# Optimization experiments

Hardware: AMD Instinct MI355X
Metric: run time of the kernel (lower is better)

The kernel has to match this reference:

```python
import jax, jax.numpy as jnp
import numpy as np

NEG_SLOPE = 0.2


def _gat_layer(x, src, dst, W, a_src, a_dst, b, n_nodes):
    # x: [N, Fin] -> h: [N, Fout]
    h = x @ W
    alpha_src = h @ a_src  # [N]
    alpha_dst = h @ a_dst  # [N]
    # per-edge attention logits (gather) + leaky relu
    e = jax.nn.leaky_relu(alpha_src[src] + alpha_dst[dst], negative_slope=NEG_SLOPE)
    # numerically-stable segment softmax over incoming edges of each dst node
    e_max = jax.ops.segment_max(e, dst, num_segments=n_nodes)
    e_exp = jnp.exp(e - e_max[dst])
    denom = jax.ops.segment_sum(e_exp, dst, num_segments=n_nodes)
    alpha = e_exp / denom[dst]  # every node has a self-loop, denom > 0
    # weighted scatter-aggregate of source features
    out = jax.ops.segment_sum(alpha[:, None] * h[src], dst, num_segments=n_nodes)
    return out + b


def setup_inputs() -> dict:
    N, E, D_EMB, D_HID = 100000, 1600000, 64, 64
    key = jax.random.key(0)
    ks = jax.random.split(key, 10)
    inp = {
        "prop_edge_index": jax.random.randint(ks[0], (2, E), 0, N, dtype=jnp.int64
                                              if jax.config.jax_enable_x64 else jnp.int32),
        "embedding": jax.random.normal(ks[1], (N, D_EMB), jnp.float32),
        "W1": jax.random.normal(ks[2], (D_EMB, D_HID), jnp.float32) / np.sqrt(D_EMB),
        "a1_src": jax.random.normal(ks[3], (D_HID,), jnp.float32) / np.sqrt(D_HID),
        "a1_dst": jax.random.normal(ks[4], (D_HID,), jnp.float32) / np.sqrt(D_HID),
        "b1": jnp.zeros((D_HID,), jnp.float32),
        "W2": jax.random.normal(ks[5], (D_HID, D_HID), jnp.float32) / np.sqrt(D_HID),
        "a2_src": jax.random.normal(ks[6], (D_HID,), jnp.float32) / np.sqrt(D_HID),
        "a2_dst": jax.random.normal(ks[7], (D_HID,), jnp.float32) / np.sqrt(D_HID),
        "b2": jnp.zeros((D_HID,), jnp.float32),
    }
    return inp


def reference(prop_edge_index, embedding, W1, a1_src, a1_dst, b1, W2, a2_src, a2_dst, b2):
    n_nodes = embedding.shape[0]
    # PyG GATConv adds self-loops by default
    loop = jnp.arange(n_nodes, dtype=prop_edge_index.dtype)
    src = jnp.concatenate([prop_edge_index[0], loop])
    dst = jnp.concatenate([prop_edge_index[1], loop])
    # dropout is identity in eval mode (args.training=False)
    x = embedding
    x = jax.nn.elu(_gat_layer(x, src, dst, W1, a1_src, a1_dst, b1, n_nodes))
    x = _gat_layer(x, src, dst, W2, a2_src, a2_dst, b2, n_nodes)
    return x
```

## Files before the change

### kernel.cpp

```cpp
#include <hip/hip_runtime.h>
#include <math.h>

#define D 64
#define NEG_SLOPE 0.2f
#define TILE 4096
#define BKT 128

__device__ __forceinline__ float lrelu(float x) { return fmaxf(x, NEG_SLOPE * x); }

__device__ __forceinline__ unsigned short f2bf(float f) {
    unsigned u = __float_as_uint(f);
    return (unsigned short)((u + 0x7fffu + ((u >> 16) & 1u)) >> 16);
}
__device__ __forceinline__ float2 bf2f2(unsigned u) {
    float2 r;
    r.x = __uint_as_float(u << 16);
    r.y = __uint_as_float(u & 0xffff0000u);
    return r;
}

__global__ __launch_bounds__(256, 4) void gemm_alpha(
    const float* __restrict__ x, const float* __restrict__ W,
    const float* __restrict__ a_src, const float* __restrict__ a_dst,
    unsigned short* __restrict__ hb, float* __restrict__ asrc,
    float* __restrict__ adst, int N) {
    __shared__ float xs[64][68];
    __shared__ float Ws[64][68];
    const int tid = threadIdx.x;
    const int r0 = blockIdx.x * 64;

    for (int i = tid; i < 4096; i += 256) {
        int k = i >> 6, c = i & 63;
        Ws[k][c] = W[i];
    }
    for (int i = tid; i < 4096; i += 256) {
        int r = i >> 6, k = i & 63;
        int gr = r0 + r;
        xs[r][k] = (gr < N) ? x[(size_t)gr * D + k] : 0.f;
    }
    __syncthreads();

    const int tx = tid & 15;
    const int ty = tid >> 4;
    float acc[4][4] = {};
#pragma unroll 4
    for (int k = 0; k < 64; k += 4) {
        float xr[4][4], wc[4][4];
#pragma unroll
        for (int i = 0; i < 4; ++i)
            *(float4*)xr[i] = *(const float4*)&xs[ty * 4 + i][k];
#pragma unroll
        for (int u = 0; u < 4; ++u)
            *(float4*)wc[u] = *(const float4*)&Ws[k + u][tx * 4];
#pragma unroll
        for (int i = 0; i < 4; ++i)
#pragma unroll
            for (int j = 0; j < 4; ++j)
#pragma unroll
                for (int u = 0; u < 4; ++u)
                    acc[i][j] = fmaf(xr[i][u], wc[u][j], acc[i][j]);
    }

#pragma unroll
    for (int i = 0; i < 4; ++i) {
        int gr = r0 + ty * 4 + i;
        if (gr < N) {
            uint2 p;
            p.x = (unsigned)f2bf(acc[i][0]) | ((unsigned)f2bf(acc[i][1]) << 16);
            p.y = (unsigned)f2bf(acc[i][2]) | ((unsigned)f2bf(acc[i][3]) << 16);
            *(uint2*)&hb[(size_t)gr * D + tx * 4] = p;
        }
    }
    float as4[4], ad4[4];
    *(float4*)as4 = *(const float4*)&a_src[tx * 4];
    *(float4*)ad4 = *(const float4*)&a_dst[tx * 4];
#pragma unroll
    for (int i = 0; i < 4; ++i) {
        float ps = 0.f, pd = 0.f;
#pragma unroll
        for (int j = 0; j < 4; ++j) {
            ps = fmaf(acc[i][j], as4[j], ps);
            pd = fmaf(acc[i][j], ad4[j], pd);
        }
#pragma unroll
        for (int off = 1; off < 16; off <<= 1) {
            ps += __shfl_xor(ps, off);
            pd += __shfl_xor(pd, off);
        }
        if (tx == 0) {
            int gr = r0 + ty * 4 + i;
            if (gr < N) { asrc[gr] = ps; adst[gr] = pd; }
        }
    }
}

__global__ void histA(const int* __restrict__ dst, int* __restrict__ mat,
                      int E, int nblkA, int NBc) {
    __shared__ int cnt[1024];
    for (int b = threadIdx.x; b < NBc; b += 256) cnt[b] = 0;
    __syncthreads();
    const int base = blockIdx.x * TILE;
    for (int j = threadIdx.x; j < TILE; j += 256) {
        int i = base + j;
        if (i < E) atomicAdd(&cnt[dst[i] >> 7], 1);
    }
    __syncthreads();
    for (int b = threadIdx.x; b < NBc; b += 256) mat[b * nblkA + blockIdx.x] = cnt[b];
}

__global__ void scan_part1(const int* __restrict__ a, int* __restrict__ bsum, int M) {
    __shared__ int s[4];
    const int lane = threadIdx.x & 63, wid = threadIdx.x >> 6;
    int base = blockIdx.x * 1024;
    int v = 0;
    for (int j = threadIdx.x; j < 1024; j += 256) {
        int i = base + j;
        v += (i < M) ? a[i] : 0;
    }
#pragma unroll
    for (int off = 32; off; off >>= 1) v += __shfl_xor(v, off);
    if (lane == 0) s[wid] = v;
    __syncthreads();
    if (threadIdx.x == 0) bsum[blockIdx.x] = s[0] + s[1] + s[2] + s[3];
}
__global__ void scan_part2(int* __restrict__ bsum, int nb) {
    const int lane = threadIdx.x;
    int running = 0;
    for (int base = 0; base < nb; base += 64) {
        int i = base + lane;
        int v = (i < nb) ? bsum[i] : 0;
        int x = v;
#pragma unroll
        for (int off = 1; off < 64; off <<= 1) {
            int y = __shfl_up(x, off);
            if (lane >= off) x += y;
        }
        if (i < nb) bsum[i] = running + x - v;
        running += __shfl(x, 63);
    }
}
__global__ void scan_part3(int* __restrict__ a, const int* __restrict__ bsum, int M) {
    __shared__ int wsum[4];
    const int lane = threadIdx.x & 63, wid = threadIdx.x >> 6;
    const int i0 = blockIdx.x * 1024 + (int)threadIdx.x * 4;
    int v[4];
#pragma unroll
    for (int u = 0; u < 4; ++u) v[u] = (i0 + u < M) ? a[i0 + u] : 0;
    int tsum = v[0] + v[1] + v[2] + v[3];
    int incl = tsum;
#pragma unroll
    for (int off = 1; off < 64; off <<= 1) {
        int y = __shfl_up(incl, off);
        if (lane >= off) incl += y;
    }
    if (lane == 63) wsum[wid] = incl;
    __syncthreads();
    int woff = 0;
    for (int w = 0; w < wid; ++w) woff += wsum[w];
    int ex = bsum[blockIdx.x] + woff + incl - tsum;
#pragma unroll
    for (int u = 0; u < 4; ++u) {
        if (i0 + u < M) a[i0 + u] = ex;
        ex += v[u];
    }
}

__global__ void scatterA(const int* __restrict__ src, const int* __restrict__ dst,
                         const int* __restrict__ mat, unsigned* __restrict__ tmp,
                         int E, int nblkA, int NBc) {
    __shared__ int cur[1024];
    for (int b = threadIdx.x; b < NBc; b += 256) cur[b] = mat[b * nblkA + blockIdx.x];
    __syncthreads();
    const int base = blockIdx.x * TILE;
    for (int j = threadIdx.x; j < TILE; j += 256) {
        int i = base + j;
        if (i < E) {
            int d = dst[i];
            int pos = atomicAdd(&cur[d >> 7], 1);
            tmp[pos] = ((unsigned)(d & (BKT - 1)) << 17) | (unsigned)src[i];
        }
    }
}

__global__ void bucket_build(const int* __restrict__ mat, const unsigned* __restrict__ tmp,
                             int* __restrict__ row, int* __restrict__ csr,
                             int N, int E, int nblkA, int NBc) {
    __shared__ int cnt[BKT];
    __shared__ int cur[BKT];
    __shared__ int wsumS[2];
    const int b = blockIdx.x;
    const int n0 = b << 7;
    const int tid = threadIdx.x;
    const int beg = mat[b * nblkA];
    const int end = (b + 1 < NBc) ? mat[(b + 1) * nblkA] : E;
    if (tid < BKT) cnt[tid] = 0;
    __syncthreads();
    for (int i = beg + tid; i < end; i += 256) atomicAdd(&cnt[tmp[i] >> 17], 1);
    __syncthreads();
    int v = (tid < BKT) ? cnt[tid] : 0;
    int x = v;
#pragma unroll
    for (int off = 1; off < 64; off <<= 1) {
        int y = __shfl_up(x, off);
        if ((tid & 63) >= off) x += y;
    }
    if (tid < BKT && (tid & 63) == 63) wsumS[tid >> 6] = x;
    __syncthreads();
    const int add = (tid >= 64 && tid < BKT) ? wsumS[0] : 0;
    const int ex = beg + add + x - v;
    if (tid < BKT) {
        const int node = n0 + tid;
        if (node < N) row[node] = ex;
        cur[tid] = ex;
    }
    if (b == NBc - 1 && tid == 0) row[N] = E;
    __syncthreads();
    for (int i = beg + tid; i < end; i += 256) {
        unsigned e = tmp[i];
        int pos = atomicAdd(&cur[e >> 17], 1);
        csr[pos] = (int)(e & 0x1FFFFu);
    }
}

__global__ __launch_bounds__(256) void aggregate(
    const int* __restrict__ row, const int* __restrict__ csr_src,
    const float* __restrict__ asrc, const float* __restrict__ adst,
    const unsigned short* __restrict__ hb, const float* __restrict__ bias,
    float* __restrict__ out, int N, int do_elu) {
    const int g = threadIdx.x >> 3;
    const int c = threadIdx.x & 7;
    const int d = blockIdx.x * 32 + g;
    if (d >= N) return;
    const int beg = row[d], end = row[d + 1];
    const float ad = adst[d];
    float dnp = __expf(lrelu(asrc[d] + ad));

    const unsigned short* hrow = hb + (c << 3);
    float acc[8];
    {
        const uint4 hv = *(const uint4*)(hrow + ((unsigned)d << 6));
        float2 p;
        p = bf2f2(hv.x); acc[0] = dnp * p.x; acc[1] = dnp * p.y;
        p = bf2f2(hv.y); acc[2] = dnp * p.x; acc[3] = dnp * p.y;
        p = bf2f2(hv.z); acc[4] = dnp * p.x; acc[5] = dnp * p.y;
        p = bf2f2(hv.w); acc[6] = dnp * p.x; acc[7] = dnp * p.y;
    }

    int i = beg;
    for (; i + 2 <= end; i += 2) {
        const int s0 = csr_src[i], s1 = csr_src[i + 1];
        const float a0 = asrc[s0], a1 = asrc[s1];
        const uint4 h0 = *(const uint4*)(hrow + ((unsigned)s0 << 6));
        const uint4 h1 = *(const uint4*)(hrow + ((unsigned)s1 << 6));
        const float w0 = __expf(lrelu(a0 + ad));
        const float w1 = __expf(lrelu(a1 + ad));
        dnp += w0 + w1;
        float2 p;
        p = bf2f2(h0.x); acc[0] = fmaf(w0, p.x, acc[0]); acc[1] = fmaf(w0, p.y, acc[1]);
        p = bf2f2(h0.y); acc[2] = fmaf(w0, p.x, acc[2]); acc[3] = fmaf(w0, p.y, acc[3]);
        p = bf2f2(h0.z); acc[4] = fmaf(w0, p.x, acc[4]); acc[5] = fmaf(w0, p.y, acc[5]);
        p = bf2f2(h0.w); acc[6] = fmaf(w0, p.x, acc[6]); acc[7] = fmaf(w0, p.y, acc[7]);
        p = bf2f2(h1.x); acc[0] = fmaf(w1, p.x, acc[0]); acc[1] = fmaf(w1, p.y, acc[1]);
        p = bf2f2(h1.y); acc[2] = fmaf(w1, p.x, acc[2]); acc[3] = fmaf(w1, p.y, acc[3]);
        p = bf2f2(h1.z); acc[4] = fmaf(w1, p.x, acc[4]); acc[5] = fmaf(w1, p.y, acc[5]);
        p = bf2f2(h1.w); acc[6] = fmaf(w1, p.x, acc[6]); acc[7] = fmaf(w1, p.y, acc[7]);
    }
    if (i < end) {
        const int s0 = csr_src[i];
        const float w0 = __expf(lrelu(asrc[s0] + ad));
        const uint4 h0 = *(const uint4*)(hrow + ((unsigned)s0 << 6));
        dnp += w0;
        float2 p;
        p = bf2f2(h0.x); acc[0] = fmaf(w0, p.x, acc[0]); acc[1] = fmaf(w0, p.y, acc[1]);
        p = bf2f2(h0.y); acc[2] = fmaf(w0, p.x, acc[2]); acc[3] = fmaf(w0, p.y, acc[3]);
        p = bf2f2(h0.z); acc[4] = fmaf(w0, p.x, acc[4]); acc[5] = fmaf(w0, p.y, acc[5]);
        p = bf2f2(h0.w); acc[6] = fmaf(w0, p.x, acc[6]); acc[7] = fmaf(w0, p.y, acc[7]);
    }

    const float inv = 1.f / dnp;
    const float4 b0 = *(const float4*)&bias[c << 3];
    const float4 b1 = *(const float4*)&bias[(c << 3) + 4];
    float v[8];
    v[0] = fmaf(acc[0], inv, b0.x); v[1] = fmaf(acc[1], inv, b0.y);
    v[2] = fmaf(acc[2], inv, b0.z); v[3] = fmaf(acc[3], inv, b0.w);
    v[4] = fmaf(acc[4], inv, b1.x); v[5] = fmaf(acc[5], inv, b1.y);
    v[6] = fmaf(acc[6], inv, b1.z); v[7] = fmaf(acc[7], inv, b1.w);
    if (do_elu) {
#pragma unroll
        for (int k = 0; k < 8; ++k) v[k] = v[k] > 0.f ? v[k] : expm1f(v[k]);
    }
    *(float4*)&out[((size_t)d << 6) + (c << 3)]     = *(float4*)&v[0];
    *(float4*)&out[((size_t)d << 6) + (c << 3) + 4] = *(float4*)&v[4];
}

extern "C" void kernel_launch(void* const* d_in, const int* in_sizes, int n_in,
                              void* d_out, int out_size, void* d_ws, size_t ws_size,
                              hipStream_t stream) {
    const int*   eidx = (const int*)d_in[0];
    const float* emb  = (const float*)d_in[1];
    const float* W1   = (const float*)d_in[2];
    const float* a1s  = (const float*)d_in[3];
    const float* a1d  = (const float*)d_in[4];
    const float* b1   = (const float*)d_in[5];
    const float* W2   = (const float*)d_in[6];
    const float* a2s  = (const float*)d_in[7];
    const float* a2d  = (const float*)d_in[8];
    const float* b2   = (const float*)d_in[9];
    float* out = (float*)d_out;

    const int E = in_sizes[0] / 2;
    const int N = in_sizes[1] / D;
    const int* src = eidx;
    const int* dst = eidx + E;

    const int nblkA = (E + TILE - 1) / TILE;
    const int NBc   = (N + BKT - 1) / BKT;
    const int M     = NBc * nblkA;
    const int nscan = (M + 1023) / 1024;

    float* ws   = (float*)d_ws;
    unsigned short* hb = (unsigned short*)ws;
    float* x1   = ws + (size_t)N * D / 2;
    float* asrc = x1 + (size_t)N * D;
    float* adst = asrc + N;
    int* row    = (int*)(adst + N);
    int* mat    = row + N + 1;
    int* msum   = mat + M;
    int* csr    = msum + nscan;
    unsigned* tmp = (unsigned*)x1;

    const int gemmBlocks = (N + 63) / 64;
    const int aggBlocks  = (N + 31) / 32;

    histA<<<nblkA, 256, 0, stream>>>(dst, mat, E, nblkA, NBc);
    scan_part1<<<nscan, 256, 0, stream>>>(mat, msum, M);
    scan_part2<<<1, 64, 0, stream>>>(msum, nscan);
    scan_part3<<<nscan, 256, 0, stream>>>(mat, msum, M);
    scatterA<<<nblkA, 256, 0, stream>>>(src, dst, mat, tmp, E, nblkA, NBc);
    bucket_build<<<NBc, 256, 0, stream>>>(mat, tmp, row, csr, N, E, nblkA, NBc);

    gemm_alpha<<<gemmBlocks, 256, 0, stream>>>(emb, W1, a1s, a1d, hb, asrc, adst, N);
    aggregate<<<aggBlocks, 256, 0, stream>>>(row, csr, asrc, adst, hb, b1, x1, N, 1);

    gemm_alpha<<<gemmBlocks, 256, 0, stream>>>(x1, W2, a2s, a2d, hb, asrc, adst, N);
    aggregate<<<aggBlocks, 256, 0, stream>>>(row, csr, asrc, adst, hb, b2, out, N, 0);
}
```

Baseline: 294.4 us.

## Use bf16 MFMA for node GEMM and store layer-1 output in bf16

Replaces the FP32 scalar-FMA 64x64 tile GEMM with bf16 MFMA 16x16x32 instructions. W and x are converted to bf16 in shared memory, and the accumulators are staged through an LDS union to produce the packed bf16 h and the attention dot products. The intermediate layer-1 activation is now written as bf16 instead of fp32, which halves its write and read traffic. This trades some precision in the GEMM inputs and intermediate activations for less compute and memory traffic in the small GEMM stages, which are a minor part next to the edge sort and aggregation.

```diff
diff --git a/kernel.cpp b/kernel.cpp
--- a/kernel.cpp
+++ b/kernel.cpp
@@ -5,6 +5,11 @@
 #define NEG_SLOPE 0.2f
 #define TILE 4096
 #define BKT 128
+#define LDK 72
+#define LDC 72
+
+typedef __attribute__((ext_vector_type(8))) short bf16x8;
+typedef __attribute__((ext_vector_type(4))) float f32x4;
 
 __device__ __forceinline__ float lrelu(float x) { return fmaxf(x, NEG_SLOPE * x); }
 
@@ -19,78 +24,100 @@
     return r;
 }
 
-__global__ __launch_bounds__(256, 4) void gemm_alpha(
-    const float* __restrict__ x, const float* __restrict__ W,
+__global__ __launch_bounds__(256) void gemm_alpha(
+    const void* __restrict__ xin, int x_is_bf16,
+    const float* __restrict__ W,
     const float* __restrict__ a_src, const float* __restrict__ a_dst,
     unsigned short* __restrict__ hb, float* __restrict__ asrc,
     float* __restrict__ adst, int N) {
-    __shared__ float xs[64][68];
-    __shared__ float Ws[64][68];
+    __shared__ union {
+        struct { unsigned short xs[64 * LDK]; unsigned short wt[64 * LDK]; } s;
+        float cs[64 * LDC];
+    } u;
     const int tid = threadIdx.x;
     const int r0 = blockIdx.x * 64;
 
-    for (int i = tid; i < 4096; i += 256) {
-        int k = i >> 6, c = i & 63;
-        Ws[k][c] = W[i];
-    }
-    for (int i = tid; i < 4096; i += 256) {
-        int r = i >> 6, k = i & 63;
-        int gr = r0 + r;
-        xs[r][k] = (gr < N) ? x[(size_t)gr * D + k] : 0.f;
-    }
-    __syncthreads();
-
-    const int tx = tid & 15;
-    const int ty = tid >> 4;
-    float acc[4][4] = {};
-#pragma unroll 4
-    for (int k = 0; k < 64; k += 4) {
-        float xr[4][4], wc[4][4];
-#pragma unroll
-        for (int i = 0; i < 4; ++i)
-            *(float4*)xr[i] = *(const float4*)&xs[ty * 4 + i][k];
-#pragma unroll
-        for (int u = 0; u < 4; ++u)
-            *(float4*)wc[u] = *(const float4*)&Ws[k + u][tx * 4];
-#pragma unroll
-        for (int i = 0; i < 4; ++i)
-#pragma unroll
-            for (int j = 0; j < 4; ++j)
-#pragma unroll
-                for (int u = 0; u < 4; ++u)
-                    acc[i][j] = fmaf(xr[i][u], wc[u][j], acc[i][j]);
-    }
-
-#pragma unroll
-    for (int i = 0; i < 4; ++i) {
-        int gr = r0 + ty * 4 + i;
+    for (int i = tid; i < 1024; i += 256) {
+        const int k = i >> 4, n0 = (i & 15) * 4;
+        const float4 w4 = *(const float4*)&W[k * 64 + n0];
+        u.s.wt[(n0 + 0) * LDK + k] = f2bf(w4.x);
+        u.s.wt[(n0 + 1) * LDK + k] = f2bf(w4.y);
+        u.s.wt[(n0 + 2) * LDK + k] = f2bf(w4.z);
+        u.s.wt[(n0 + 3) * LDK + k] = f2bf(w4.w);
+    }
+    if (x_is_bf16) {
+        const unsigned short* xb = (const unsigned short*)xin;
+        for (int i = tid; i < 1024; i += 256) {
+            const int r = i >> 4, c0 = (i & 15) * 4;
+            const int gr = r0 + r;
+            uint2 v = make_uint2(0u, 0u);
+            if (gr < N) v = *(const uint2*)&xb[(size_t)gr * D + c0];
+            *(uint2*)&u.s.xs[r * LDK + c0] = v;
+        }
+    } else {
+        const float* xf = (const float*)xin;
+        for (int i = tid; i < 1024; i += 256) {
+            const int r = i >> 4, c0 = (i & 15) * 4;
+            const int gr = r0 + r;
+            float4 v = make_float4(0.f, 0.f, 0.f, 0.f);
+            if (gr < N) v = *(const float4*)&xf[(size_t)gr * D + c0];
+            unsigned short q[4] = {f2bf(v.x), f2bf(v.y), f2bf(v.z), f2bf(v.w)};
+            *(uint2*)&u.s.xs[r * LDK + c0] = *(uint2*)q;
+        }
+    }
+    __syncthreads();
+
+    const int wv = tid >> 6, lane = tid & 63;
+    const int m = lane & 15, quad = lane >> 4;
+    const int rw = wv * 16;
+    bf16x8 afr0 = *(const bf16x8*)&u.s.xs[(rw + m) * LDK + quad * 8];
+    bf16x8 afr1 = *(const bf16x8*)&u.s.xs[(rw + m) * LDK + 32 + quad * 8];
+    f32x4 acc[4];
+#pragma unroll
+    for (int nt = 0; nt < 4; ++nt) {
+        f32x4 a = {0.f, 0.f, 0.f, 0.f};
+        const bf16x8 b0 = *(const bf16x8*)&u.s.wt[(nt * 16 + m) * LDK + quad * 8];
+        const bf16x8 b1 = *(const bf16x8*)&u.s.wt[(nt * 16 + m) * LDK + 32 + quad * 8];
+        a = __builtin_amdgcn_mfma_f32_16x16x32_bf16(afr0, b0, a, 0, 0, 0);
+        a = __builtin_amdgcn_mfma_f32_16x16x32_bf16(afr1, b1, a, 0, 0, 0);
+        acc[nt] = a;
+    }
+    __syncthreads();
+#pragma unroll
+    for (int nt = 0; nt < 4; ++nt)
+#pragma unroll
+        for (int reg = 0; reg < 4; ++reg)
+            u.cs[(rw + quad * 4 + reg) * LDC + nt * 16 + m] = acc[nt][reg];
+    __syncthreads();
+
+    {
+        const int r = tid >> 2, cseg = (tid & 3) * 16;
+        const int gr = r0 + r;
+        float vals[16];
+#pragma unroll
+        for (int q4 = 0; q4 < 4; ++q4)
+            *(float4*)&vals[q4 * 4] = *(const float4*)&u.cs[r * LDC + cseg + q4 * 4];
         if (gr < N) {
-            uint2 p;
-            p.x = (unsigned)f2bf(acc[i][0]) | ((unsigned)f2bf(acc[i][1]) << 16);
-            p.y = (unsigned)f2bf(acc[i][2]) | ((unsigned)f2bf(acc[i][3]) << 16);
-            *(uint2*)&hb[(size_t)gr * D + tx * 4] = p;
-        }
-    }
-    float as4[4], ad4[4];
-    *(float4*)as4 = *(const float4*)&a_src[tx * 4];
-    *(float4*)ad4 = *(const float4*)&a_dst[tx * 4];
-#pragma unroll
-    for (int i = 0; i < 4; ++i) {
+            unsigned pk[8];
+#pragma unroll
+            for (int j = 0; j < 8; ++j)
+                pk[j] = (unsigned)f2bf(vals[2 * j]) | ((unsigned)f2bf(vals[2 * j + 1]) << 16);
+            *(uint4*)&hb[(size_t)gr * D + cseg] = *(uint4*)&pk[0];
+            *(uint4*)&hb[(size_t)gr * D + cseg + 8] = *(uint4*)&pk[4];
+        }
         float ps = 0.f, pd = 0.f;
 #pragma unroll
-        for (int j = 0; j < 4; ++j) {
-            ps = fmaf(acc[i][j], as4[j], ps);
-            pd = fmaf(acc[i][j], ad4[j], pd);
-        }
-#pragma unroll
-        for (int off = 1; off < 16; off <<= 1) {
-            ps += __shfl_xor(ps, off);
-            pd += __shfl_xor(pd, off);
-        }
-        if (tx == 0) {
-            int gr = r0 + ty * 4 + i;
-            if (gr < N) { asrc[gr] = ps; adst[gr] = pd; }
-        }
+        for (int q4 = 0; q4 < 4; ++q4) {
+            const float4 as4 = *(const float4*)&a_src[cseg + q4 * 4];
+            const float4 ad4 = *(const float4*)&a_dst[cseg + q4 * 4];
+            ps = fmaf(vals[q4 * 4 + 0], as4.x, ps); pd = fmaf(vals[q4 * 4 + 0], ad4.x, pd);
+            ps = fmaf(vals[q4 * 4 + 1], as4.y, ps); pd = fmaf(vals[q4 * 4 + 1], ad4.y, pd);
+            ps = fmaf(vals[q4 * 4 + 2], as4.z, ps); pd = fmaf(vals[q4 * 4 + 2], ad4.z, pd);
+            ps = fmaf(vals[q4 * 4 + 3], as4.w, ps); pd = fmaf(vals[q4 * 4 + 3], ad4.w, pd);
+        }
+        ps += __shfl_xor(ps, 1); ps += __shfl_xor(ps, 2);
+        pd += __shfl_xor(pd, 1); pd += __shfl_xor(pd, 2);
+        if ((tid & 3) == 0 && gr < N) { asrc[gr] = ps; adst[gr] = pd; }
     }
 }
 
@@ -226,7 +253,7 @@
     const int* __restrict__ row, const int* __restrict__ csr_src,
     const float* __restrict__ asrc, const float* __restrict__ adst,
     const unsigned short* __restrict__ hb, const float* __restrict__ bias,
-    float* __restrict__ out, int N, int do_elu) {
+    void* __restrict__ outp, int N, int do_elu, int out_bf16) {
     const int g = threadIdx.x >> 3;
     const int c = threadIdx.x & 7;
     const int d = blockIdx.x * 32 + g;
@@ -289,8 +316,17 @@
 #pragma unroll
         for (int k = 0; k < 8; ++k) v[k] = v[k] > 0.f ? v[k] : expm1f(v[k]);
     }
-    *(float4*)&out[((size_t)d << 6) + (c << 3)]     = *(float4*)&v[0];
-    *(float4*)&out[((size_t)d << 6) + (c << 3) + 4] = *(float4*)&v[4];
+    if (out_bf16) {
+        unsigned pk[4];
+#pragma unroll
+        for (int j = 0; j < 4; ++j)
+            pk[j] = (unsigned)f2bf(v[2 * j]) | ((unsigned)f2bf(v[2 * j + 1]) << 16);
+        *(uint4*)((unsigned short*)outp + ((size_t)d << 6) + (c << 3)) = *(uint4*)pk;
+    } else {
+        float* out = (float*)outp;
+        *(float4*)&out[((size_t)d << 6) + (c << 3)]     = *(float4*)&v[0];
+        *(float4*)&out[((size_t)d << 6) + (c << 3) + 4] = *(float4*)&v[4];
+    }
 }
 
 extern "C" void kernel_launch(void* const* d_in, const int* in_sizes, int n_in,
@@ -318,16 +354,15 @@
     const int M     = NBc * nblkA;
     const int nscan = (M + 1023) / 1024;
 
-    float* ws   = (float*)d_ws;
-    unsigned short* hb = (unsigned short*)ws;
-    float* x1   = ws + (size_t)N * D / 2;
-    float* asrc = x1 + (size_t)N * D;
+    unsigned short* hb  = (unsigned short*)d_ws;
+    unsigned short* x1b = hb + (size_t)N * D;
+    float* asrc = (float*)(x1b + (size_t)N * D);
     float* adst = asrc + N;
     int* row    = (int*)(adst + N);
     int* mat    = row + N + 1;
     int* msum   = mat + M;
     int* csr    = msum + nscan;
-    unsigned* tmp = (unsigned*)x1;
+    unsigned* tmp = (unsigned*)x1b;
 
     const int gemmBlocks = (N + 63) / 64;
     const int aggBlocks  = (N + 31) / 32;
@@ -339,9 +374,9 @@
     scatterA<<<nblkA, 256, 0, stream>>>(src, dst, mat, tmp, E, nblkA, NBc);
     bucket_build<<<NBc, 256, 0, stream>>>(mat, tmp, row, csr, N, E, nblkA, NBc);
 
-    gemm_alpha<<<gemmBlocks, 256, 0, stream>>>(emb, W1, a1s, a1d, hb, asrc, adst, N);
-    aggregate<<<aggBlocks, 256, 0, stream>>>(row, csr, asrc, adst, hb, b1, x1, N, 1);
-
-    gemm_alpha<<<gemmBlocks, 256, 0, stream>>>(x1, W2, a2s, a2d, hb, asrc, adst, N);
-    aggregate<<<aggBlocks, 256, 0, stream>>>(row, csr, asrc, adst, hb, b2, out, N, 0);
-}
+    gemm_alpha<<<gemmBlocks, 256, 0, stream>>>(emb, 0, W1, a1s, a1d, hb, asrc, adst, N);
+    aggregate<<<aggBlocks, 256, 0, stream>>>(row, csr, asrc, adst, hb, b1, x1b, N, 1, 1);
+
+    gemm_alpha<<<gemmBlocks, 256, 0, stream>>>(x1b, 1, W2, a2s, a2d, hb, asrc, adst, N);
+    aggregate<<<aggBlocks, 256, 0, stream>>>(row, csr, asrc, adst, hb, b2, out, N, 0, 0);
+}
```

New measurement: 267.5 us. -9.1%, faster.
